# Performance work log

Hardware: AMD Instinct MI355X
Metric: run time of the kernel (lower is better)

The kernel has to match this reference:

```python
import jax, jax.numpy as jnp
import numpy as np

B, S, D = 4, 2048, 1024
E, TOPK, F = 8, 2, 4096


def setup_inputs() -> dict:
    key = jax.random.key(0)
    ks = jax.random.split(key, 6)
    hidden_states = jax.random.normal(ks[0], (B, S, D), dtype=jnp.float32)
    gate_w = jax.random.normal(ks[1], (D, E), dtype=jnp.float32) * (1.0 / np.sqrt(D))
    w1 = jax.random.normal(ks[2], (E, D, F), dtype=jnp.float32) * (1.0 / np.sqrt(D))
    b1 = jnp.zeros((E, F), dtype=jnp.float32)
    w2 = jax.random.normal(ks[3], (E, F, D), dtype=jnp.float32) * (1.0 / np.sqrt(F))
    b2 = jnp.zeros((E, D), dtype=jnp.float32)
    return {"hidden_states": hidden_states, "gate_w": gate_w,
            "w1": w1, "b1": b1, "w2": w2, "b2": b2}


def reference(hidden_states, gate_w, w1, b1, w2, b2):
    b, s, d = hidden_states.shape
    x = hidden_states.reshape(-1, d)                      # [T, D]
    router_logits = x @ gate_w                            # [T, E]
    routing_weights = jax.nn.softmax(router_logits, axis=1)
    topk_w, selected = jax.lax.top_k(routing_weights, TOPK)  # [T, K]
    topk_w = topk_w / topk_w.sum(axis=-1, keepdims=True)
    topk_w = topk_w.astype(hidden_states.dtype)
    # dense combine weights: zero for non-selected experts -> identical math
    # to the per-expert gather/scatter-add loop in the original module.
    combine = (jax.nn.one_hot(selected, E, dtype=topk_w.dtype)
               * topk_w[..., None]).sum(axis=1)           # [T, E]
    # grouped FFN experts over all tokens (dense dispatch)
    h = jnp.einsum('td,edf->tef', x, w1) + b1[None]       # [T, E, F]
    h = jax.nn.gelu(h)
    y = jnp.einsum('tef,efd->ted', h, w2) + b2[None]      # [T, E, D]
    out = jnp.einsum('ted,te->td', y, combine)            # [T, D]
    return out.reshape(b, s, d)
```

## Files before the change

### kernel.cpp

```cpp
#include <hip/hip_runtime.h>

#define T_TOK 8192
#define DDIM  1024
#define NEXP  8
#define FDIM  4096
#define BM    128
#define BK    64
#define SLOT_CAP (T_TOK*2 + NEXP*BM)

using short8  = __attribute__((ext_vector_type(8))) short;
using floatx4 = __attribute__((ext_vector_type(4))) float;

__device__ __forceinline__ unsigned short f32_to_bf16(float f) {
    unsigned int u = __float_as_uint(f);
    u = (u + 0x7FFFu + ((u >> 16) & 1u)) >> 16;
    return (unsigned short)u;
}

__global__ void router_kernel(const float* __restrict__ x, const float* __restrict__ gw,
                              int* __restrict__ tk_e, float* __restrict__ tk_g,
                              unsigned short* __restrict__ xb) {
    const int wave = threadIdx.x >> 6, lane = threadIdx.x & 63;
    const int t = blockIdx.x * 4 + wave;
    const float* xr = x + (size_t)t * DDIM;
    unsigned short* xbr = xb + (size_t)t * DDIM;
    float acc[8] = {0.f,0.f,0.f,0.f,0.f,0.f,0.f,0.f};
    for (int i = lane; i < DDIM; i += 64) {
        float xv = xr[i];
        xbr[i] = f32_to_bf16(xv);
        const float4* g4 = (const float4*)(gw + i * NEXP);
        float4 a = g4[0], b = g4[1];
        acc[0] += xv*a.x; acc[1] += xv*a.y; acc[2] += xv*a.z; acc[3] += xv*a.w;
        acc[4] += xv*b.x; acc[5] += xv*b.y; acc[6] += xv*b.z; acc[7] += xv*b.w;
    }
    #pragma unroll
    for (int s = 32; s > 0; s >>= 1)
        #pragma unroll
        for (int e = 0; e < 8; ++e)
            acc[e] += __shfl_xor(acc[e], s, 64);
    if (lane == 0) {
        int e0 = 0; float v0 = acc[0];
        #pragma unroll
        for (int e = 1; e < 8; ++e) if (acc[e] > v0) { v0 = acc[e]; e0 = e; }
        int e1 = -1; float v1 = -1e30f;
        #pragma unroll
        for (int e = 0; e < 8; ++e) if (e != e0 && acc[e] > v1) { v1 = acc[e]; e1 = e; }
        float g0 = 1.0f / (1.0f + expf(v1 - v0));
        tk_e[t*2] = e0;  tk_e[t*2+1] = e1;
        tk_g[t*2] = g0;  tk_g[t*2+1] = 1.0f - g0;
    }
}

__global__ void sortscatter_kernel(const int* __restrict__ tk_e, int* __restrict__ offsets,
                                   int* __restrict__ perm_token, int* __restrict__ tok2slot) {
    __shared__ int cnt[NEXP];
    __shared__ int off_s[NEXP + 1];
    __shared__ int cur[NEXP];
    const int tid = threadIdx.x;
    if (tid < NEXP) cnt[tid] = 0;
    __syncthreads();
    for (int i = tid; i < 2 * T_TOK; i += 1024)
        atomicAdd(&cnt[tk_e[i]], 1);
    __syncthreads();
    if (tid == 0) {
        int o = 0;
        for (int e = 0; e < NEXP; ++e) {
            off_s[e] = o; cur[e] = 0;
            o += (cnt[e] + BM - 1) & ~(BM - 1);
        }
        off_s[NEXP] = o;
    }
    __syncthreads();
    if (tid <= NEXP) offsets[tid] = off_s[tid];
    for (int i = tid; i < 2 * T_TOK; i += 1024) {
        int e = tk_e[i];
        int slot = off_s[e] + atomicAdd(&cur[e], 1);
        perm_token[slot] = i >> 1;
        tok2slot[i] = slot;
    }
    __syncthreads();
    #pragma unroll
    for (int e = 0; e < NEXP; ++e) {
        int base = off_s[e] + cnt[e];
        int pad  = off_s[e + 1] - base;
        for (int i = tid; i < pad; i += 1024) perm_token[base + i] = 0;
    }
}

__global__ void transpose_cvt2_kernel(const float* __restrict__ w1, const float* __restrict__ w2,
                                      unsigned short* __restrict__ w1T, unsigned short* __restrict__ w2T) {
    const int z = blockIdx.y;
    const bool is1 = z < NEXP;
    const int e = is1 ? z : z - NEXP;
    const int C = is1 ? FDIM : DDIM;
    const int cshift = is1 ? 6 : 4;
    const int R = is1 ? DDIM : FDIM;
    const float* w = (is1 ? w1 : w2) + (size_t)e * DDIM * FDIM;
    unsigned short* o = (is1 ? w1T : w2T) + (size_t)e * DDIM * FDIM;
    const int t = blockIdx.x;
    const int c0 = (t & ((C >> 6) - 1)) * 64, r0 = (t >> cshift) * 64;
    __shared__ float tile[64][65];
    const int l = threadIdx.x & 15, row = threadIdx.x >> 4;
    #pragma unroll
    for (int j = 0; j < 4; ++j) {
        int r = row + j * 16;
        float4 v = *(const float4*)(w + (size_t)(r0 + r) * C + c0 + l * 4);
        tile[r][l*4+0] = v.x; tile[r][l*4+1] = v.y; tile[r][l*4+2] = v.z; tile[r][l*4+3] = v.w;
    }
    __syncthreads();
    #pragma unroll
    for (int j = 0; j < 4; ++j) {
        int c = row + j * 16;
        ushort4 v;
        v.x = f32_to_bf16(tile[l*4+0][c]);
        v.y = f32_to_bf16(tile[l*4+1][c]);
        v.z = f32_to_bf16(tile[l*4+2][c]);
        v.w = f32_to_bf16(tile[l*4+3][c]);
        *(ushort4*)(o + (size_t)(c0 + c) * R + r0 + l * 4) = v;
    }
}

#define STAGE(AS, BS, KOFF) do {                                                            \
    _Pragma("unroll")                                                                       \
    for (int r = 0; r < 4; ++r) {                                                           \
        __builtin_amdgcn_global_load_lds(                                                   \
            (const __attribute__((address_space(1))) void*)(aptr[r] + (KOFF)),              \
            (__attribute__((address_space(3))) void*)((char*)(AS) + (r * 32 + wave * 8) * 128), \
            16, 0, 0);                                                                      \
        __builtin_amdgcn_global_load_lds(                                                   \
            (const __attribute__((address_space(1))) void*)(bptr[r] + (KOFF)),              \
            (__attribute__((address_space(3))) void*)((char*)(BS) + (r * 32 + wave * 8) * 128), \
            16, 0, 0);                                                                      \
    } } while (0)

#define COMPUTE(AS, BS) do {                                                                \
    _Pragma("unroll")                                                                       \
    for (int kh = 0; kh < 2; ++kh) {                                                        \
        short8 af[4], bfr[4];                                                               \
        _Pragma("unroll")                                                                   \
        for (int im = 0; im < 4; ++im) {                                                    \
            int m = wm * 64 + im * 16 + l15;                                                \
            af[im] = *(const short8*)((const char*)(AS) + m * 128 + (((kh * 4 + quad) ^ l7) << 4)); \
        }                                                                                   \
        _Pragma("unroll")                                                                   \
        for (int in = 0; in < 4; ++in) {                                                    \
            int n = wn * 64 + in * 16 + l15;                                                \
            bfr[in] = *(const short8*)((const char*)(BS) + n * 128 + (((kh * 4 + quad) ^ l7) << 4)); \
        }                                                                                   \
        _Pragma("unroll")                                                                   \
        for (int im = 0; im < 4; ++im)                                                      \
            _Pragma("unroll")                                                               \
            for (int in = 0; in < 4; ++in)                                                  \
                acc[im][in] = __builtin_amdgcn_mfma_f32_16x16x32_bf16(af[im], bfr[in], acc[im][in], 0, 0, 0); \
    } } while (0)

__global__ __launch_bounds__(256, 3) void gemm1_kernel(
    const unsigned short* __restrict__ xb, const unsigned short* __restrict__ w1T,
    const float* __restrict__ b1, const int* __restrict__ perm_token,
    const int* __restrict__ offsets, unsigned short* __restrict__ h) {
    __shared__ __align__(16) unsigned short As[BM * BK];
    __shared__ __align__(16) unsigned short Bs[BM * BK];
    const int p = blockIdx.x;
    const int q = p >> 3;
    const int nt = q & 31;
    const int mt = ((q >> 5) << 3) | (p & 7);
    const int row0 = mt * BM;
    if (row0 >= offsets[NEXP]) return;
    const int n0 = nt * BM;
    int e = 0;
    while (e < NEXP - 1 && offsets[e + 1] <= row0) ++e;
    const int lane = threadIdx.x & 63, wave = threadIdx.x >> 6;
    const int srow = lane >> 3;
    const int scol = (lane & 7) ^ srow;
    const unsigned short* aptr[4];
    const unsigned short* bptr[4];
    #pragma unroll
    for (int r = 0; r < 4; ++r) {
        int arow = r * 32 + wave * 8 + srow;
        int tok = perm_token[row0 + arow];
        aptr[r] = xb + (size_t)tok * DDIM + scol * 8;
        int brow = n0 + r * 32 + wave * 8 + srow;
        bptr[r] = w1T + ((size_t)e * FDIM + brow) * DDIM + scol * 8;
    }
    const int wm = wave >> 1, wn = wave & 1;
    const int l15 = lane & 15, quad = lane >> 4, l7 = lane & 7;
    floatx4 acc[4][4];
    #pragma unroll
    for (int im = 0; im < 4; ++im)
        #pragma unroll
        for (int in = 0; in < 4; ++in)
            acc[im][in] = (floatx4){0.f, 0.f, 0.f, 0.f};

    #pragma unroll 1
    for (int kk = 0; kk < DDIM; kk += BK) {
        __syncthreads();
        STAGE(As, Bs, kk);
        asm volatile("s_waitcnt vmcnt(0)" ::: "memory");
        __syncthreads();
        COMPUTE(As, Bs);
    }
    #pragma unroll
    for (int im = 0; im < 4; ++im) {
        int mbase = row0 + wm * 64 + im * 16 + quad * 4;
        #pragma unroll
        for (int r = 0; r < 4; ++r) {
            #pragma unroll
            for (int in = 0; in < 4; ++in) {
                int n = n0 + wn * 64 + in * 16 + l15;
                float z = acc[im][in][r] + b1[e * FDIM + n];
                float u = __expf(1.5957691216057308f * (z + 0.044715f * z * z * z));
                float t = 1.0f - __fdividef(2.0f, u + 1.0f);
                float g = 0.5f * z * (1.0f + t);
                h[(size_t)(mbase + r) * FDIM + n] = f32_to_bf16(g);
            }
        }
    }
}

__global__ __launch_bounds__(256, 3) void gemm2_kernel(
    const unsigned short* __restrict__ h, const unsigned short* __restrict__ w2T,
    const float* __restrict__ b2, const int* __restrict__ offsets,
    float* __restrict__ y) {
    __shared__ __align__(16) unsigned short As[BM * BK];
    __shared__ __align__(16) unsigned short Bs[BM * BK];
    const int p = blockIdx.x;
    const int q = p >> 3;
    const int nt = q & 7;
    const int mt = ((q >> 3) << 3) | (p & 7);
    const int row0 = mt * BM;
    if (row0 >= offsets[NEXP]) return;
    const int n0 = nt * BM;
    int e = 0;
    while (e < NEXP - 1 && offsets[e + 1] <= row0) ++e;
    const int lane = threadIdx.x & 63, wave = threadIdx.x >> 6;
    const int srow = lane >> 3;
    const int scol = (lane & 7) ^ srow;
    const unsigned short* aptr[4];
    const unsigned short* bptr[4];
    #pragma unroll
    for (int r = 0; r < 4; ++r) {
        int arow = r * 32 + wave * 8 + srow;
        aptr[r] = h + (size_t)(row0 + arow) * FDIM + scol * 8;
        int brow = n0 + r * 32 + wave * 8 + srow;
        bptr[r] = w2T + ((size_t)e * DDIM + brow) * FDIM + scol * 8;
    }
    const int wm = wave >> 1, wn = wave & 1;
    const int l15 = lane & 15, quad = lane >> 4, l7 = lane & 7;
    floatx4 acc[4][4];
    #pragma unroll
    for (int im = 0; im < 4; ++im)
        #pragma unroll
        for (int in = 0; in < 4; ++in)
            acc[im][in] = (floatx4){0.f, 0.f, 0.f, 0.f};

    #pragma unroll 1
    for (int kk = 0; kk < FDIM; kk += BK) {
        __syncthreads();
        STAGE(As, Bs, kk);
        asm volatile("s_waitcnt vmcnt(0)" ::: "memory");
        __syncthreads();
        COMPUTE(As, Bs);
    }
    #pragma unroll
    for (int im = 0; im < 4; ++im) {
        int mbase = row0 + wm * 64 + im * 16 + quad * 4;
        #pragma unroll
        for (int r = 0; r < 4; ++r) {
            #pragma unroll
            for (int in = 0; in < 4; ++in) {
                int n = n0 + wn * 64 + in * 16 + l15;
                y[(size_t)(mbase + r) * DDIM + n] = acc[im][in][r] + b2[e * DDIM + n];
            }
        }
    }
}

__global__ void combine_kernel(const float* __restrict__ y, const int* __restrict__ tok2slot,
                               const float* __restrict__ tk_g, float* __restrict__ out) {
    const int t = blockIdx.x;
    const int s0 = tok2slot[2 * t], s1 = tok2slot[2 * t + 1];
    const float g0 = tk_g[2 * t], g1 = tk_g[2 * t + 1];
    float4 a = ((const float4*)(y + (size_t)s0 * DDIM))[threadIdx.x];
    float4 b = ((const float4*)(y + (size_t)s1 * DDIM))[threadIdx.x];
    float4 o;
    o.x = g0 * a.x + g1 * b.x;  o.y = g0 * a.y + g1 * b.y;
    o.z = g0 * a.z + g1 * b.z;  o.w = g0 * a.w + g1 * b.w;
    ((float4*)(out + (size_t)t * DDIM))[threadIdx.x] = o;
}

extern "C" void kernel_launch(void* const* d_in, const int* in_sizes, int n_in,
                              void* d_out, int out_size, void* d_ws, size_t ws_size,
                              hipStream_t stream) {
    (void)in_sizes; (void)n_in; (void)ws_size; (void)out_size;
    const float* x  = (const float*)d_in[0];
    const float* gw = (const float*)d_in[1];
    const float* w1 = (const float*)d_in[2];
    const float* b1 = (const float*)d_in[3];
    const float* w2 = (const float*)d_in[4];
    const float* b2 = (const float*)d_in[5];
    float* out = (float*)d_out;

    char* ws = (char*)d_ws;
    size_t off = 0;
    unsigned short* xb  = (unsigned short*)(ws + off); off += (size_t)T_TOK * DDIM * 2;
    unsigned short* w1T = (unsigned short*)(ws + off); off += (size_t)NEXP * DDIM * FDIM * 2;
    unsigned short* w2T = (unsigned short*)(ws + off); off += (size_t)NEXP * DDIM * FDIM * 2;
    unsigned short* h   = (unsigned short*)(ws + off); off += (size_t)SLOT_CAP * FDIM * 2;
    float* y = (float*)d_ws;
    int*   meta       = (int*)(ws + off);
    int*   perm_token = meta;
    int*   offsets    = meta + SLOT_CAP;
    int*   tk_e       = offsets + NEXP + 1;
    float* tk_g       = (float*)(tk_e + 2 * T_TOK);
    int*   tok2slot   = (int*)(tk_g + 2 * T_TOK);

    router_kernel<<<T_TOK / 4, 256, 0, stream>>>(x, gw, tk_e, tk_g, xb);
    sortscatter_kernel<<<1, 1024, 0, stream>>>(tk_e, offsets, perm_token, tok2slot);
    dim3 gt(1024, 2 * NEXP);
    transpose_cvt2_kernel<<<gt, 256, 0, stream>>>(w1, w2, w1T, w2T);

    gemm1_kernel<<<(SLOT_CAP / BM) * (FDIM / BM), 256, 0, stream>>>(xb, w1T, b1, perm_token, offsets, h);
    gemm2_kernel<<<(SLOT_CAP / BM) * (DDIM / BM), 256, 0, stream>>>(h, w2T, b2, offsets, y);
    combine_kernel<<<T_TOK, 256, 0, stream>>>(y, tok2slot, tk_g, out);
}
```

Before: 742.0 us.

## Pipeline expert GEMMs with a three-stage LDS ring and BK=32

```diff
diff --git a/kernel.cpp b/kernel.cpp
--- a/kernel.cpp
+++ b/kernel.cpp
@@ -5,7 +5,7 @@
 #define NEXP  8
 #define FDIM  4096
 #define BM    128
-#define BK    64
+#define BK    32
 #define SLOT_CAP (T_TOK*2 + NEXP*BM)
 
 using short8  = __attribute__((ext_vector_type(8))) short;
@@ -120,46 +120,62 @@
     }
 }
 
-#define STAGE(AS, BS, KOFF) do {                                                            \
+
+#define STAGE2(AD, BD, KOFF) do {                                                           \
     _Pragma("unroll")                                                                       \
-    for (int r = 0; r < 4; ++r) {                                                           \
+    for (int r_ = 0; r_ < 2; ++r_) {                                                        \
         __builtin_amdgcn_global_load_lds(                                                   \
-            (const __attribute__((address_space(1))) void*)(aptr[r] + (KOFF)),              \
-            (__attribute__((address_space(3))) void*)((char*)(AS) + (r * 32 + wave * 8) * 128), \
+            (const __attribute__((address_space(1))) void*)(aptr[r_] + (KOFF)),             \
+            (__attribute__((address_space(3))) void*)((char*)(AD) + (r_ * 64 + wave * 16) * 64), \
             16, 0, 0);                                                                      \
         __builtin_amdgcn_global_load_lds(                                                   \
-            (const __attribute__((address_space(1))) void*)(bptr[r] + (KOFF)),              \
-            (__attribute__((address_space(3))) void*)((char*)(BS) + (r * 32 + wave * 8) * 128), \
+            (const __attribute__((address_space(1))) void*)(bptr[r_] + (KOFF)),             \
+            (__attribute__((address_space(3))) void*)((char*)(BD) + (r_ * 64 + wave * 16) * 64), \
             16, 0, 0);                                                                      \
     } } while (0)
 
-#define COMPUTE(AS, BS) do {                                                                \
+#define COMPUTE2(AD, BD) do {                                                               \
+    short8 af[4], bfr[4];                                                                   \
     _Pragma("unroll")                                                                       \
-    for (int kh = 0; kh < 2; ++kh) {                                                        \
-        short8 af[4], bfr[4];                                                               \
+    for (int im = 0; im < 4; ++im) {                                                        \
+        int m = wm * 64 + im * 16 + l15;                                                    \
+        af[im] = *(const short8*)((const char*)(AD) + m * 64 + ((quad ^ ((l15 >> 1) & 3)) << 4)); \
+    }                                                                                       \
+    _Pragma("unroll")                                                                       \
+    for (int in = 0; in < 4; ++in) {                                                        \
+        int n = wn * 64 + in * 16 + l15;                                                    \
+        bfr[in] = *(const short8*)((const char*)(BD) + n * 64 + ((quad ^ ((l15 >> 1) & 3)) << 4)); \
+    }                                                                                       \
+    _Pragma("unroll")                                                                       \
+    for (int im = 0; im < 4; ++im)                                                          \
         _Pragma("unroll")                                                                   \
-        for (int im = 0; im < 4; ++im) {                                                    \
-            int m = wm * 64 + im * 16 + l15;                                                \
-            af[im] = *(const short8*)((const char*)(AS) + m * 128 + (((kh * 4 + quad) ^ l7) << 4)); \
-        }                                                                                   \
-        _Pragma("unroll")                                                                   \
-        for (int in = 0; in < 4; ++in) {                                                    \
-            int n = wn * 64 + in * 16 + l15;                                                \
-            bfr[in] = *(const short8*)((const char*)(BS) + n * 128 + (((kh * 4 + quad) ^ l7) << 4)); \
-        }                                                                                   \
-        _Pragma("unroll")                                                                   \
-        for (int im = 0; im < 4; ++im)                                                      \
-            _Pragma("unroll")                                                               \
-            for (int in = 0; in < 4; ++in)                                                  \
-                acc[im][in] = __builtin_amdgcn_mfma_f32_16x16x32_bf16(af[im], bfr[in], acc[im][in], 0, 0, 0); \
-    } } while (0)
+        for (int in = 0; in < 4; ++in)                                                      \
+            acc[im][in] = __builtin_amdgcn_mfma_f32_16x16x32_bf16(af[im], bfr[in], acc[im][in], 0, 0, 0); \
+    } while (0)
+
+#define GEMM_RING_LOOP(NT) do {                                                             \
+    STAGE2(&As[0][0], &Bs[0][0], 0);                                                        \
+    STAGE2(&As[1][0], &Bs[1][0], BK);                                                       \
+    int s0 = 0, s1 = 1, s2 = 2;                                                             \
+    _Pragma("unroll 1")                                                                     \
+    for (int t = 0; t < (NT) - 1; ++t) {                                                    \
+        asm volatile("s_waitcnt vmcnt(4)" ::: "memory");                                    \
+        __builtin_amdgcn_s_barrier();                                                       \
+        if (t + 2 < (NT)) STAGE2(&As[s2][0], &Bs[s2][0], (t + 2) * BK);                     \
+        COMPUTE2(&As[s0][0], &Bs[s0][0]);                                                   \
+        int tmp = s0; s0 = s1; s1 = s2; s2 = tmp;                                           \
+    }                                                                                       \
+    asm volatile("s_waitcnt vmcnt(0)" ::: "memory");                                        \
+    __builtin_amdgcn_s_barrier();                                                           \
+    COMPUTE2(&As[s0][0], &Bs[s0][0]);                                                       \
+} while (0)
 
 __global__ __launch_bounds__(256, 3) void gemm1_kernel(
     const unsigned short* __restrict__ xb, const unsigned short* __restrict__ w1T,
     const float* __restrict__ b1, const int* __restrict__ perm_token,
     const int* __restrict__ offsets, unsigned short* __restrict__ h) {
-    __shared__ __align__(16) unsigned short As[BM * BK];
-    __shared__ __align__(16) unsigned short Bs[BM * BK];
+    __shared__ __align__(16) unsigned short As[3][BM * BK];
+    __shared__ __align__(16) unsigned short Bs[3][BM * BK];
     const int p = blockIdx.x;
     const int q = p >> 3;
     const int nt = q & 31;
@@ -170,20 +186,20 @@
     int e = 0;
     while (e < NEXP - 1 && offsets[e + 1] <= row0) ++e;
     const int lane = threadIdx.x & 63, wave = threadIdx.x >> 6;
-    const int srow = lane >> 3;
-    const int scol = (lane & 7) ^ srow;
-    const unsigned short* aptr[4];
-    const unsigned short* bptr[4];
-    #pragma unroll
-    for (int r = 0; r < 4; ++r) {
-        int arow = r * 32 + wave * 8 + srow;
+    const int srow = lane >> 2;
+    const int scol = (lane & 3) ^ ((lane >> 3) & 3);
+    const unsigned short* aptr[2];
+    const unsigned short* bptr[2];
+    #pragma unroll
+    for (int r = 0; r < 2; ++r) {
+        int arow = r * 64 + wave * 16 + srow;
         int tok = perm_token[row0 + arow];
         aptr[r] = xb + (size_t)tok * DDIM + scol * 8;
-        int brow = n0 + r * 32 + wave * 8 + srow;
+        int brow = n0 + r * 64 + wave * 16 + srow;
         bptr[r] = w1T + ((size_t)e * FDIM + brow) * DDIM + scol * 8;
     }
     const int wm = wave >> 1, wn = wave & 1;
-    const int l15 = lane & 15, quad = lane >> 4, l7 = lane & 7;
+    const int l15 = lane & 15, quad = lane >> 4;
     floatx4 acc[4][4];
     #pragma unroll
     for (int im = 0; im < 4; ++im)
@@ -191,14 +207,8 @@
         for (int in = 0; in < 4; ++in)
             acc[im][in] = (floatx4){0.f, 0.f, 0.f, 0.f};
 
-    #pragma unroll 1
-    for (int kk = 0; kk < DDIM; kk += BK) {
-        __syncthreads();
-        STAGE(As, Bs, kk);
-        asm volatile("s_waitcnt vmcnt(0)" ::: "memory");
-        __syncthreads();
-        COMPUTE(As, Bs);
-    }
+    GEMM_RING_LOOP(DDIM / BK);
+
     #pragma unroll
     for (int im = 0; im < 4; ++im) {
         int mbase = row0 + wm * 64 + im * 16 + quad * 4;
@@ -221,8 +231,8 @@
     const unsigned short* __restrict__ h, const unsigned short* __restrict__ w2T,
     const float* __restrict__ b2, const int* __restrict__ offsets,
     float* __restrict__ y) {
-    __shared__ __align__(16) unsigned short As[BM * BK];
-    __shared__ __align__(16) unsigned short Bs[BM * BK];
+    __shared__ __align__(16) unsigned short As[3][BM * BK];
+    __shared__ __align__(16) unsigned short Bs[3][BM * BK];
     const int p = blockIdx.x;
     const int q = p >> 3;
     const int nt = q & 7;
@@ -233,19 +243,19 @@
     int e = 0;
     while (e < NEXP - 1 && offsets[e + 1] <= row0) ++e;
     const int lane = threadIdx.x & 63, wave = threadIdx.x >> 6;
-    const int srow = lane >> 3;
-    const int scol = (lane & 7) ^ srow;
-    const unsigned short* aptr[4];
-    const unsigned short* bptr[4];
-    #pragma unroll
-    for (int r = 0; r < 4; ++r) {
-        int arow = r * 32 + wave * 8 + srow;
+    const int srow = lane >> 2;
+    const int scol = (lane & 3) ^ ((lane >> 3) & 3);
+    const unsigned short* aptr[2];
+    const unsigned short* bptr[2];
+    #pragma unroll
+    for (int r = 0; r < 2; ++r) {
+        int arow = r * 64 + wave * 16 + srow;
         aptr[r] = h + (size_t)(row0 + arow) * FDIM + scol * 8;
-        int brow = n0 + r * 32 + wave * 8 + srow;
+        int brow = n0 + r * 64 + wave * 16 + srow;
         bptr[r] = w2T + ((size_t)e * DDIM + brow) * FDIM + scol * 8;
     }
     const int wm = wave >> 1, wn = wave & 1;
-    const int l15 = lane & 15, quad = lane >> 4, l7 = lane & 7;
+    const int l15 = lane & 15, quad = lane >> 4;
     floatx4 acc[4][4];
     #pragma unroll
     for (int im = 0; im < 4; ++im)
@@ -253,14 +263,8 @@
         for (int in = 0; in < 4; ++in)
             acc[im][in] = (floatx4){0.f, 0.f, 0.f, 0.f};
 
-    #pragma unroll 1
-    for (int kk = 0; kk < FDIM; kk += BK) {
-        __syncthreads();
-        STAGE(As, Bs, kk);
-        asm volatile("s_waitcnt vmcnt(0)" ::: "memory");
-        __syncthreads();
-        COMPUTE(As, Bs);
-    }
+    GEMM_RING_LOOP(FDIM / BK);
+
     #pragma unroll
     for (int im = 0; im < 4; ++im) {
         int mbase = row0 + wm * 64 + im * 16 + quad * 4;
```

Measured after the change: 807.8 us. 8.9% more time.
